# Optimization experiments

Measured on AMD Instinct MI355X. Metric: run time of the kernel, lower is better.

## Reference

```python
import jax, jax.numpy as jnp
import numpy as np

N_EMBD = 384
SEQ_LEN = 256
B = 512


def setup_inputs() -> dict:
    key = jax.random.key(0)
    ks = jax.random.split(key, 5)
    s = 1.0 / np.sqrt(N_EMBD)
    x = jax.random.normal(ks[0], (B, SEQ_LEN, N_EMBD), dtype=jnp.float32)
    W_qkv = jax.random.uniform(ks[1], (N_EMBD, 3 * N_EMBD), jnp.float32, -s, s)
    b_qkv = jax.random.uniform(ks[2], (3 * N_EMBD,), jnp.float32, -s, s)
    W_proj = jax.random.uniform(ks[3], (N_EMBD, N_EMBD), jnp.float32, -s, s)
    b_proj = jax.random.uniform(ks[4], (N_EMBD,), jnp.float32, -s, s)
    return {"x": x, "W_qkv": W_qkv, "b_qkv": b_qkv, "W_proj": W_proj, "b_proj": b_proj}


def reference(x, W_qkv, b_qkv, W_proj, b_proj):
    B_, T, C = x.shape
    qkv = jnp.einsum('btc,cd->btd', x, W_qkv) + b_qkv  # [B,T,3C]
    q, k, v = jnp.split(qkv, 3, axis=-1)
    # single-head attention, scaled by full embed dim C (as in source)
    att = jnp.einsum('btc,bsc->bts', q, k) / jnp.sqrt(jnp.float32(C))  # [B,T,T]
    causal = jnp.tril(jnp.ones((T, T), dtype=bool))
    att = jnp.where(causal, att, -jnp.inf)
    att = jax.nn.softmax(att, axis=-1)
    out = jnp.einsum('bts,bsc->btc', att, v)  # [B,T,C]
    return jnp.einsum('btc,cd->btd', out, W_proj) + b_proj
```

## Files before the change

kernel.cpp:

```cpp
#include <hip/hip_runtime.h>
#include <math.h>

#define TSEQ 256
#define CEMB 384
#define QK_LD 768
#define QKV_N 1152

typedef short short8 __attribute__((ext_vector_type(8)));
typedef short short4v __attribute__((ext_vector_type(4)));
typedef float f32x4 __attribute__((ext_vector_type(4)));

static __device__ __forceinline__ short f2bf(float f) {
    union { float f; unsigned u; } a;
    a.f = f;
    unsigned u = a.u + 0x7fffu + ((a.u >> 16) & 1u);
    return (short)(u >> 16);
}

static __device__ __forceinline__ void gload_lds16(const unsigned short* g,
                                                   unsigned short* l) {
    __builtin_amdgcn_global_load_lds(
        (const __attribute__((address_space(1))) unsigned int*)g,
        (__attribute__((address_space(3))) unsigned int*)l, 16, 0, 0);
}

__global__ __launch_bounds__(256) void cast_x_kernel(
    const float* __restrict__ x, unsigned short* __restrict__ xb, int n8)
{
    int i = blockIdx.x * 256 + threadIdx.x;
    const int stride = gridDim.x * 256;
    for (; i < n8; i += stride) {
        const float* s = x + (size_t)i * 8;
        float4 a = *(const float4*)(s);
        float4 c = *(const float4*)(s + 4);
        short8 o;
        o[0] = f2bf(a.x); o[1] = f2bf(a.y); o[2] = f2bf(a.z); o[3] = f2bf(a.w);
        o[4] = f2bf(c.x); o[5] = f2bf(c.y); o[6] = f2bf(c.z); o[7] = f2bf(c.w);
        *(short8*)(xb + (size_t)i * 8) = o;
    }
}

__global__ __launch_bounds__(256) void cast_wt_kernel(
    const float* __restrict__ W, unsigned short* __restrict__ Wt, int K, int N)
{
    int i = blockIdx.x * 256 + threadIdx.x;
    if (i < K * N) {
        int n = i / K;
        int k = i - n * K;
        Wt[i] = (unsigned short)f2bf(W[(size_t)k * N + n]);
    }
}

template <int MODE>
__global__ __launch_bounds__(256) void gemm_bf16_kernel(
    const unsigned short* __restrict__ A, const unsigned short* __restrict__ Bt,
    const float* __restrict__ bias, void* __restrict__ Cout,
    unsigned short* __restrict__ Vt, int M, int N, int K)
{
    __shared__ unsigned short As[2][128 * 32];
    __shared__ unsigned short Bs[2][128 * 32];

    const int tid  = threadIdx.x;
    const int wave = tid >> 6;
    const int lane = tid & 63;
    const int quad = lane >> 4;
    const int l16  = lane & 15;
    const int wr   = wave >> 1;
    const int wc   = wave & 1;

    const int gx  = gridDim.x;
    const int nwg = gridDim.x * gridDim.y;
    int bid = blockIdx.y * gx + blockIdx.x;
    if ((nwg & 7) == 0) bid = (bid & 7) * (nwg >> 3) + (bid >> 3);
    const int n0 = (bid % gx) * 128;
    const int m0 = (bid / gx) * 128;

    const int srow = tid >> 2;
    const int scol = (tid & 3) * 8;
    const unsigned short* Abase = A  + (size_t)(m0 + srow) * K + scol;
    const unsigned short* Bbase = Bt + (size_t)(n0 + srow) * K + scol;
    const int woff = wave << 9;

    f32x4 acc[4][4];
    #pragma unroll
    for (int mi = 0; mi < 4; ++mi)
        #pragma unroll
        for (int ni = 0; ni < 4; ++ni) acc[mi][ni] = (f32x4){0.f, 0.f, 0.f, 0.f};

    gload_lds16(Abase, &As[0][woff]);
    gload_lds16(Abase + (size_t)64 * K, &As[0][2048 + woff]);
    gload_lds16(Bbase, &Bs[0][woff]);
    gload_lds16(Bbase + (size_t)64 * K, &Bs[0][2048 + woff]);
    __syncthreads();

    int cur = 0;
    for (int kk = 32; kk < K; kk += 32) {
        gload_lds16(Abase + kk, &As[cur ^ 1][woff]);
        gload_lds16(Abase + (size_t)64 * K + kk, &As[cur ^ 1][2048 + woff]);
        gload_lds16(Bbase + kk, &Bs[cur ^ 1][woff]);
        gload_lds16(Bbase + (size_t)64 * K + kk, &Bs[cur ^ 1][2048 + woff]);

        short8 af[4], bfr[4];
        #pragma unroll
        for (int mi = 0; mi < 4; ++mi)
            af[mi] = *(const short8*)&As[cur][(wr * 64 + mi * 16 + l16) * 32 + quad * 8];
        #pragma unroll
        for (int ni = 0; ni < 4; ++ni)
            bfr[ni] = *(const short8*)&Bs[cur][(wc * 64 + ni * 16 + l16) * 32 + quad * 8];
        #pragma unroll
        for (int mi = 0; mi < 4; ++mi)
            #pragma unroll
            for (int ni = 0; ni < 4; ++ni)
                acc[mi][ni] = __builtin_amdgcn_mfma_f32_16x16x32_bf16(
                    af[mi], bfr[ni], acc[mi][ni], 0, 0, 0);

        __syncthreads();
        cur ^= 1;
    }
    {
        short8 af[4], bfr[4];
        #pragma unroll
        for (int mi = 0; mi < 4; ++mi)
            af[mi] = *(const short8*)&As[cur][(wr * 64 + mi * 16 + l16) * 32 + quad * 8];
        #pragma unroll
        for (int ni = 0; ni < 4; ++ni)
            bfr[ni] = *(const short8*)&Bs[cur][(wc * 64 + ni * 16 + l16) * 32 + quad * 8];
        #pragma unroll
        for (int mi = 0; mi < 4; ++mi)
            #pragma unroll
            for (int ni = 0; ni < 4; ++ni)
                acc[mi][ni] = __builtin_amdgcn_mfma_f32_16x16x32_bf16(
                    af[mi], bfr[ni], acc[mi][ni], 0, 0, 0);
    }

    if (MODE == 1 && n0 >= 768) {
        #pragma unroll
        for (int ni = 0; ni < 4; ++ni) {
            const int n = n0 + wc * 64 + ni * 16 + l16;
            const float bv = bias[n];
            const int c = n - 768;
            #pragma unroll
            for (int mi = 0; mi < 4; ++mi) {
                const int m = m0 + wr * 64 + mi * 16 + quad * 4;
                const int bb = m >> 8;
                const int t  = m & 255;
                short4v o;
                #pragma unroll
                for (int r = 0; r < 4; ++r)
                    o[r] = f2bf(acc[mi][ni][r] + bv);
                *(short4v*)(Vt + ((size_t)bb * CEMB + c) * TSEQ + t) = o;
            }
        }
        return;
    }

    #pragma unroll
    for (int ni = 0; ni < 4; ++ni) {
        const int n = n0 + wc * 64 + ni * 16 + l16;
        const float bv = bias[n];
        #pragma unroll
        for (int mi = 0; mi < 4; ++mi) {
            #pragma unroll
            for (int r = 0; r < 4; ++r) {
                const int m = m0 + wr * 64 + mi * 16 + quad * 4 + r;
                float v = acc[mi][ni][r] + bv;
                if (MODE == 1)
                    ((unsigned short*)Cout)[(size_t)m * QK_LD + n] = (unsigned short)f2bf(v);
                else
                    ((float*)Cout)[(size_t)m * N + n] = v;
            }
        }
    }
}

__global__ __launch_bounds__(64) void attn_mfma_kernel(
    const unsigned short* __restrict__ QKb, const unsigned short* __restrict__ Vt,
    unsigned short* __restrict__ Ob)
{
    const int nwg = gridDim.x;
    int bid = blockIdx.x;
    bid = (bid & 7) * (nwg >> 3) + (bid >> 3);
    const int b  = bid >> 4;
    const int st = bid & 15;

    const int lane = threadIdx.x;
    const int quad = lane >> 4;
    const int l16  = lane & 15;
    const int Q0   = st * 16;
    const int NT   = st + 1;
    const int NKT32  = (NT + 1) >> 1;
    const int kcnt   = NT * 16;
    const int padcnt = NKT32 * 32;

    __shared__ unsigned short Pw[16 * 264];

    const float scale = 0.051031036307982884f;

    const unsigned short* qbase = QKb + ((size_t)b * TSEQ + Q0) * QK_LD;
    short8 qf[12];
    #pragma unroll
    for (int f = 0; f < 12; ++f)
        qf[f] = *(const short8*)(qbase + (size_t)l16 * QK_LD + f * 32 + quad * 8);

    f32x4 s[16];
    #pragma unroll
    for (int t = 0; t < 16; ++t) s[t] = (f32x4){0.f, 0.f, 0.f, 0.f};

    const unsigned short* kB = QKb + (size_t)b * TSEQ * QK_LD + CEMB;
    #pragma unroll
    for (int t = 0; t < 16; ++t) {
        if (t <= st) {
            const unsigned short* kp = kB + (size_t)(t * 16 + l16) * QK_LD + quad * 8;
            #pragma unroll
            for (int f = 0; f < 12; ++f) {
                short8 kf = *(const short8*)(kp + f * 32);
                s[t] = __builtin_amdgcn_mfma_f32_16x16x32_bf16(qf[f], kf, s[t], 0, 0, 0);
            }
        }
    }

    float mt[4] = {-1e30f, -1e30f, -1e30f, -1e30f};
    #pragma unroll
    for (int t = 0; t < 16; ++t) {
        if (t <= st) {
            #pragma unroll
            for (int r = 0; r < 4; ++r) {
                const int qrow = Q0 + quad * 4 + r;
                float v = s[t][r] * scale;
                if (t * 16 + l16 > qrow) v = -1e30f;
                s[t][r] = v;
                mt[r] = fmaxf(mt[r], v);
            }
        }
    }
    #pragma unroll
    for (int off = 1; off <= 8; off <<= 1)
        #pragma unroll
        for (int r = 0; r < 4; ++r)
            mt[r] = fmaxf(mt[r], __shfl_xor(mt[r], off));

    float lr[4] = {0.f, 0.f, 0.f, 0.f};
    #pragma unroll
    for (int t = 0; t < 16; ++t) {
        if (t <= st) {
            #pragma unroll
            for (int r = 0; r < 4; ++r) {
                float p = __expf(s[t][r] - mt[r]);
                s[t][r] = p;
                lr[r] += p;
            }
        }
    }
    #pragma unroll
    for (int off = 1; off <= 8; off <<= 1)
        #pragma unroll
        for (int r = 0; r < 4; ++r)
            lr[r] += __shfl_xor(lr[r], off);
    float inv[4];
    #pragma unroll
    for (int r = 0; r < 4; ++r) inv[r] = 1.f / lr[r];

    #pragma unroll
    for (int t = 0; t < 16; ++t) {
        if (t * 16 < padcnt) {
            #pragma unroll
            for (int r = 0; r < 4; ++r) {
                float pv = (t <= st) ? s[t][r] : 0.f;
                Pw[(quad * 4 + r) * 264 + t * 16 + l16] = (unsigned short)f2bf(pv);
            }
        }
    }
    __asm__ __volatile__("s_waitcnt lgkmcnt(0)" ::: "memory");

    short8 pf[8];
    #pragma unroll
    for (int kt = 0; kt < 8; ++kt)
        if (kt < NKT32)
            pf[kt] = *(const short8*)(Pw + (size_t)l16 * 264 + kt * 32 + quad * 8);

    const unsigned short* vB = Vt + (size_t)b * CEMB * TSEQ;
    unsigned short* obase = Ob + ((size_t)b * TSEQ + Q0) * CEMB;
    #pragma unroll 4
    for (int ct = 0; ct < 24; ++ct) {
        const unsigned short* vp = vB + (size_t)(ct * 16 + l16) * TSEQ + quad * 8;
        f32x4 o = (f32x4){0.f, 0.f, 0.f, 0.f};
        #pragma unroll
        for (int kt = 0; kt < 8; ++kt) {
            if (kt < NKT32) {
                short8 vf = *(const short8*)(vp + kt * 32);
                o = __builtin_amdgcn_mfma_f32_16x16x32_bf16(pf[kt], vf, o, 0, 0, 0);
            }
        }
        #pragma unroll
        for (int r = 0; r < 4; ++r)
            obase[(size_t)(quad * 4 + r) * CEMB + ct * 16 + l16] =
                (unsigned short)f2bf(o[r] * inv[r]);
    }
}

extern "C" void kernel_launch(void* const* d_in, const int* in_sizes, int n_in,
                              void* d_out, int out_size, void* d_ws, size_t ws_size,
                              hipStream_t stream)
{
    const float* x      = (const float*)d_in[0];
    const float* W_qkv  = (const float*)d_in[1];
    const float* b_qkv  = (const float*)d_in[2];
    const float* W_proj = (const float*)d_in[3];
    const float* b_proj = (const float*)d_in[4];
    float* out = (float*)d_out;

    const int Btot = 512;
    const size_t xb_pb  = (size_t)TSEQ * CEMB * 2;
    const size_t qkb_pb = (size_t)TSEQ * QK_LD * 2;
    const size_t vt_pb  = (size_t)TSEQ * CEMB * 2;
    const size_t ob_pb  = (size_t)TSEQ * CEMB * 2;
    const size_t per_batch = xb_pb + qkb_pb + vt_pb + ob_pb;
    const size_t wq_sz = (size_t)CEMB * QKV_N * 2;
    const size_t wp_sz = (size_t)CEMB * CEMB * 2;
    const size_t fixed = wq_sz + wp_sz;

    size_t avail = (ws_size > fixed) ? (ws_size - fixed) : 0;
    int chunk = (int)(avail / per_batch);
    if (chunk > Btot) chunk = Btot;
    if (chunk < 1) chunk = 1;

    char* p = (char*)d_ws;
    unsigned short* xb  = (unsigned short*)p;  p += xb_pb * chunk;
    unsigned short* QKb = (unsigned short*)p;  p += qkb_pb * chunk;
    unsigned short* Vt  = (unsigned short*)p;  p += vt_pb * chunk;
    unsigned short* Ob  = (unsigned short*)p;  p += ob_pb * chunk;
    unsigned short* Wqt = (unsigned short*)p;  p += wq_sz;
    unsigned short* Wpt = (unsigned short*)p;

    cast_wt_kernel<<<(CEMB * QKV_N + 255) / 256, 256, 0, stream>>>(
        W_qkv, Wqt, CEMB, QKV_N);
    cast_wt_kernel<<<(CEMB * CEMB + 255) / 256, 256, 0, stream>>>(
        W_proj, Wpt, CEMB, CEMB);

    for (int b0 = 0; b0 < Btot; b0 += chunk) {
        int cb = (chunk < Btot - b0) ? chunk : (Btot - b0);
        int Mc = cb * TSEQ;

        int n8 = Mc * CEMB / 8;
        int gx = (n8 + 255) / 256;
        if (gx > 2048) gx = 2048;
        cast_x_kernel<<<gx, 256, 0, stream>>>(
            x + (size_t)b0 * TSEQ * CEMB, xb, n8);

        gemm_bf16_kernel<1><<<dim3(QKV_N / 128, Mc / 128), 256, 0, stream>>>(
            xb, Wqt, b_qkv, QKb, Vt, Mc, QKV_N, CEMB);

        attn_mfma_kernel<<<dim3(16 * cb), 64, 0, stream>>>(QKb, Vt, Ob);

        gemm_bf16_kernel<0><<<dim3(CEMB / 128, Mc / 128), 256, 0, stream>>>(
            Ob, Wpt, b_proj, out + (size_t)b0 * TSEQ * CEMB, nullptr, Mc, CEMB, CEMB);
    }
}
```

Measured before the change: 1.046 ms.

## Split fused attention into tiled QK GEMM, row softmax, and PV GEMM kernels

Replaces the single-wave per-16-row attention kernel with three kernels: a 128x128 LDS-tiled, double-buffered QK^T GEMM that skips the fully masked upper tile, a row softmax writing bf16 probabilities and inverse sums, and a tiled PV GEMM that limits K to the causal extent. The goal is better operand reuse through LDS and higher MFMA utilization than the old kernel, which reread K and V straight from global memory per 16-row tile. The cost is an fp32 score matrix and a bf16 P matrix round-tripping through global memory, plus extra launches and a smaller batch chunk from the larger workspace.

```diff
diff --git a/kernel.cpp b/kernel.cpp
--- a/kernel.cpp
+++ b/kernel.cpp
@@ -173,128 +173,242 @@
     }
 }
 
-__global__ __launch_bounds__(64) void attn_mfma_kernel(
-    const unsigned short* __restrict__ QKb, const unsigned short* __restrict__ Vt,
-    unsigned short* __restrict__ Ob)
-{
-    const int nwg = gridDim.x;
-    int bid = blockIdx.x;
-    bid = (bid & 7) * (nwg >> 3) + (bid >> 3);
-    const int b  = bid >> 4;
-    const int st = bid & 15;
-
-    const int lane = threadIdx.x;
+__global__ __launch_bounds__(256) void qk_gemm_kernel(
+    const unsigned short* __restrict__ QKb, float* __restrict__ S)
+{
+    const int tt = blockIdx.x;
+    const int b  = blockIdx.y;
+    const int ti = (tt >= 1) ? 1 : 0;
+    const int tj = (tt == 2) ? 1 : 0;
+    const int m0 = ti * 128, n0 = tj * 128;
+
+    __shared__ unsigned short As[2][128 * 32];
+    __shared__ unsigned short Bs[2][128 * 32];
+
+    const int tid  = threadIdx.x;
+    const int wave = tid >> 6;
+    const int lane = tid & 63;
     const int quad = lane >> 4;
     const int l16  = lane & 15;
-    const int Q0   = st * 16;
-    const int NT   = st + 1;
-    const int NKT32  = (NT + 1) >> 1;
-    const int kcnt   = NT * 16;
-    const int padcnt = NKT32 * 32;
-
-    __shared__ unsigned short Pw[16 * 264];
-
-    const float scale = 0.051031036307982884f;
-
-    const unsigned short* qbase = QKb + ((size_t)b * TSEQ + Q0) * QK_LD;
-    short8 qf[12];
-    #pragma unroll
-    for (int f = 0; f < 12; ++f)
-        qf[f] = *(const short8*)(qbase + (size_t)l16 * QK_LD + f * 32 + quad * 8);
-
-    f32x4 s[16];
-    #pragma unroll
-    for (int t = 0; t < 16; ++t) s[t] = (f32x4){0.f, 0.f, 0.f, 0.f};
-
-    const unsigned short* kB = QKb + (size_t)b * TSEQ * QK_LD + CEMB;
-    #pragma unroll
-    for (int t = 0; t < 16; ++t) {
-        if (t <= st) {
-            const unsigned short* kp = kB + (size_t)(t * 16 + l16) * QK_LD + quad * 8;
-            #pragma unroll
-            for (int f = 0; f < 12; ++f) {
-                short8 kf = *(const short8*)(kp + f * 32);
-                s[t] = __builtin_amdgcn_mfma_f32_16x16x32_bf16(qf[f], kf, s[t], 0, 0, 0);
+    const int wr   = wave >> 1;
+    const int wc   = wave & 1;
+
+    const int srow = tid >> 2;
+    const int scol = (tid & 3) * 8;
+    const unsigned short* Abase = QKb + ((size_t)b * TSEQ + m0 + srow) * QK_LD + scol;
+    const unsigned short* Bbase = QKb + ((size_t)b * TSEQ + n0 + srow) * QK_LD + CEMB + scol;
+    const int woff = wave << 9;
+
+    f32x4 acc[4][4];
+    #pragma unroll
+    for (int mi = 0; mi < 4; ++mi)
+        #pragma unroll
+        for (int ni = 0; ni < 4; ++ni) acc[mi][ni] = (f32x4){0.f, 0.f, 0.f, 0.f};
+
+    gload_lds16(Abase, &As[0][woff]);
+    gload_lds16(Abase + (size_t)64 * QK_LD, &As[0][2048 + woff]);
+    gload_lds16(Bbase, &Bs[0][woff]);
+    gload_lds16(Bbase + (size_t)64 * QK_LD, &Bs[0][2048 + woff]);
+    __syncthreads();
+
+    int cur = 0;
+    for (int kk = 32; kk < CEMB; kk += 32) {
+        gload_lds16(Abase + kk, &As[cur ^ 1][woff]);
+        gload_lds16(Abase + (size_t)64 * QK_LD + kk, &As[cur ^ 1][2048 + woff]);
+        gload_lds16(Bbase + kk, &Bs[cur ^ 1][woff]);
+        gload_lds16(Bbase + (size_t)64 * QK_LD + kk, &Bs[cur ^ 1][2048 + woff]);
+
+        short8 af[4], bfr[4];
+        #pragma unroll
+        for (int mi = 0; mi < 4; ++mi)
+            af[mi] = *(const short8*)&As[cur][(wr * 64 + mi * 16 + l16) * 32 + quad * 8];
+        #pragma unroll
+        for (int ni = 0; ni < 4; ++ni)
+            bfr[ni] = *(const short8*)&Bs[cur][(wc * 64 + ni * 16 + l16) * 32 + quad * 8];
+        #pragma unroll
+        for (int mi = 0; mi < 4; ++mi)
+            #pragma unroll
+            for (int ni = 0; ni < 4; ++ni)
+                acc[mi][ni] = __builtin_amdgcn_mfma_f32_16x16x32_bf16(
+                    af[mi], bfr[ni], acc[mi][ni], 0, 0, 0);
+
+        __syncthreads();
+        cur ^= 1;
+    }
+    {
+        short8 af[4], bfr[4];
+        #pragma unroll
+        for (int mi = 0; mi < 4; ++mi)
+            af[mi] = *(const short8*)&As[cur][(wr * 64 + mi * 16 + l16) * 32 + quad * 8];
+        #pragma unroll
+        for (int ni = 0; ni < 4; ++ni)
+            bfr[ni] = *(const short8*)&Bs[cur][(wc * 64 + ni * 16 + l16) * 32 + quad * 8];
+        #pragma unroll
+        for (int mi = 0; mi < 4; ++mi)
+            #pragma unroll
+            for (int ni = 0; ni < 4; ++ni)
+                acc[mi][ni] = __builtin_amdgcn_mfma_f32_16x16x32_bf16(
+                    af[mi], bfr[ni], acc[mi][ni], 0, 0, 0);
+    }
+
+    float* Sb = S + (size_t)b * TSEQ * TSEQ;
+    #pragma unroll
+    for (int ni = 0; ni < 4; ++ni) {
+        const int n = n0 + wc * 64 + ni * 16 + l16;
+        #pragma unroll
+        for (int mi = 0; mi < 4; ++mi) {
+            #pragma unroll
+            for (int r = 0; r < 4; ++r) {
+                const int m = m0 + wr * 64 + mi * 16 + quad * 4 + r;
+                Sb[(size_t)m * TSEQ + n] = acc[mi][ni][r];
             }
         }
     }
-
-    float mt[4] = {-1e30f, -1e30f, -1e30f, -1e30f};
-    #pragma unroll
-    for (int t = 0; t < 16; ++t) {
-        if (t <= st) {
-            #pragma unroll
-            for (int r = 0; r < 4; ++r) {
-                const int qrow = Q0 + quad * 4 + r;
-                float v = s[t][r] * scale;
-                if (t * 16 + l16 > qrow) v = -1e30f;
-                s[t][r] = v;
-                mt[r] = fmaxf(mt[r], v);
+}
+
+__global__ __launch_bounds__(256) void softmax_rows_kernel(
+    const float* __restrict__ S, unsigned short* __restrict__ P,
+    float* __restrict__ Linv)
+{
+    const int b    = blockIdx.y;
+    const int t    = blockIdx.x * 4 + (threadIdx.x >> 6);
+    const int lane = threadIdx.x & 63;
+    const int col  = lane * 4;
+    const int Kcov = ((t >> 7) + 1) * 128;
+    const float scale = 0.051031036307982884f;
+
+    const float* sp = S + ((size_t)b * TSEQ + t) * TSEQ;
+    float v[4];
+    if (col < Kcov) {
+        float4 sv = *(const float4*)(sp + col);
+        v[0] = (col + 0 <= t) ? sv.x * scale : -1e30f;
+        v[1] = (col + 1 <= t) ? sv.y * scale : -1e30f;
+        v[2] = (col + 2 <= t) ? sv.z * scale : -1e30f;
+        v[3] = (col + 3 <= t) ? sv.w * scale : -1e30f;
+    } else {
+        v[0] = v[1] = v[2] = v[3] = -1e30f;
+    }
+
+    float m = fmaxf(fmaxf(v[0], v[1]), fmaxf(v[2], v[3]));
+    #pragma unroll
+    for (int off = 1; off <= 32; off <<= 1)
+        m = fmaxf(m, __shfl_xor(m, off));
+
+    float p[4];
+    float s = 0.f;
+    #pragma unroll
+    for (int j = 0; j < 4; ++j) {
+        p[j] = __expf(v[j] - m);
+        s += p[j];
+    }
+    #pragma unroll
+    for (int off = 1; off <= 32; off <<= 1)
+        s += __shfl_xor(s, off);
+
+    if (lane == 0) Linv[(size_t)b * TSEQ + t] = 1.f / s;
+
+    if (col < Kcov) {
+        short4v o;
+        #pragma unroll
+        for (int j = 0; j < 4; ++j) o[j] = f2bf(p[j]);
+        *(short4v*)(P + ((size_t)b * TSEQ + t) * TSEQ + col) = o;
+    }
+}
+
+__global__ __launch_bounds__(256) void pv_gemm_kernel(
+    const unsigned short* __restrict__ P, const unsigned short* __restrict__ Vt,
+    const float* __restrict__ Linv, unsigned short* __restrict__ Ob)
+{
+    const int tt = blockIdx.x;
+    const int b  = blockIdx.y;
+    const int ti = tt / 3;
+    const int tj = tt - ti * 3;
+    const int m0 = ti * 128, n0 = tj * 128;
+    const int Kext = (ti + 1) * 128;
+
+    __shared__ unsigned short As[2][128 * 32];
+    __shared__ unsigned short Bs[2][128 * 32];
+
+    const int tid  = threadIdx.x;
+    const int wave = tid >> 6;
+    const int lane = tid & 63;
+    const int quad = lane >> 4;
+    const int l16  = lane & 15;
+    const int wr   = wave >> 1;
+    const int wc   = wave & 1;
+
+    const int srow = tid >> 2;
+    const int scol = (tid & 3) * 8;
+    const unsigned short* Abase = P  + ((size_t)b * TSEQ + m0 + srow) * TSEQ + scol;
+    const unsigned short* Bbase = Vt + ((size_t)b * CEMB + n0 + srow) * TSEQ + scol;
+    const int woff = wave << 9;
+
+    f32x4 acc[4][4];
+    #pragma unroll
+    for (int mi = 0; mi < 4; ++mi)
+        #pragma unroll
+        for (int ni = 0; ni < 4; ++ni) acc[mi][ni] = (f32x4){0.f, 0.f, 0.f, 0.f};
+
+    gload_lds16(Abase, &As[0][woff]);
+    gload_lds16(Abase + (size_t)64 * TSEQ, &As[0][2048 + woff]);
+    gload_lds16(Bbase, &Bs[0][woff]);
+    gload_lds16(Bbase + (size_t)64 * TSEQ, &Bs[0][2048 + woff]);
+    __syncthreads();
+
+    int cur = 0;
+    for (int kk = 32; kk < Kext; kk += 32) {
+        gload_lds16(Abase + kk, &As[cur ^ 1][woff]);
+        gload_lds16(Abase + (size_t)64 * TSEQ + kk, &As[cur ^ 1][2048 + woff]);
+        gload_lds16(Bbase + kk, &Bs[cur ^ 1][woff]);
+        gload_lds16(Bbase + (size_t)64 * TSEQ + kk, &Bs[cur ^ 1][2048 + woff]);
+
+        short8 af[4], bfr[4];
+        #pragma unroll
+        for (int mi = 0; mi < 4; ++mi)
+            af[mi] = *(const short8*)&As[cur][(wr * 64 + mi * 16 + l16) * 32 + quad * 8];
+        #pragma unroll
+        for (int ni = 0; ni < 4; ++ni)
+            bfr[ni] = *(const short8*)&Bs[cur][(wc * 64 + ni * 16 + l16) * 32 + quad * 8];
+        #pragma unroll
+        for (int mi = 0; mi < 4; ++mi)
+            #pragma unroll
+            for (int ni = 0; ni < 4; ++ni)
+                acc[mi][ni] = __builtin_amdgcn_mfma_f32_16x16x32_bf16(
+                    af[mi], bfr[ni], acc[mi][ni], 0, 0, 0);
+
+        __syncthreads();
+        cur ^= 1;
+    }
+    {
+        short8 af[4], bfr[4];
+        #pragma unroll
+        for (int mi = 0; mi < 4; ++mi)
+            af[mi] = *(const short8*)&As[cur][(wr * 64 + mi * 16 + l16) * 32 + quad * 8];
+        #pragma unroll
+        for (int ni = 0; ni < 4; ++ni)
+            bfr[ni] = *(const short8*)&Bs[cur][(wc * 64 + ni * 16 + l16) * 32 + quad * 8];
+        #pragma unroll
+        for (int mi = 0; mi < 4; ++mi)
+            #pragma unroll
+            for (int ni = 0; ni < 4; ++ni)
+                acc[mi][ni] = __builtin_amdgcn_mfma_f32_16x16x32_bf16(
+                    af[mi], bfr[ni], acc[mi][ni], 0, 0, 0);
+    }
+
+    const float* lv = Linv + (size_t)b * TSEQ;
+    unsigned short* ob = Ob + (size_t)b * TSEQ * CEMB;
+    #pragma unroll
+    for (int mi = 0; mi < 4; ++mi) {
+        #pragma unroll
+        for (int r = 0; r < 4; ++r) {
+            const int m = m0 + wr * 64 + mi * 16 + quad * 4 + r;
+            const float inv = lv[m];
+            #pragma unroll
+            for (int ni = 0; ni < 4; ++ni) {
+                const int n = n0 + wc * 64 + ni * 16 + l16;
+                ob[(size_t)m * CEMB + n] = (unsigned short)f2bf(acc[mi][ni][r] * inv);
             }
         }
-    }
-    #pragma unroll
-    for (int off = 1; off <= 8; off <<= 1)
-        #pragma unroll
-        for (int r = 0; r < 4; ++r)
-            mt[r] = fmaxf(mt[r], __shfl_xor(mt[r], off));
-
-    float lr[4] = {0.f, 0.f, 0.f, 0.f};
-    #pragma unroll
-    for (int t = 0; t < 16; ++t) {
-        if (t <= st) {
-            #pragma unroll
-            for (int r = 0; r < 4; ++r) {
-                float p = __expf(s[t][r] - mt[r]);
-                s[t][r] = p;
-                lr[r] += p;
-            }
-        }
-    }
-    #pragma unroll
-    for (int off = 1; off <= 8; off <<= 1)
-        #pragma unroll
-        for (int r = 0; r < 4; ++r)
-            lr[r] += __shfl_xor(lr[r], off);
-    float inv[4];
-    #pragma unroll
-    for (int r = 0; r < 4; ++r) inv[r] = 1.f / lr[r];
-
-    #pragma unroll
-    for (int t = 0; t < 16; ++t) {
-        if (t * 16 < padcnt) {
-            #pragma unroll
-            for (int r = 0; r < 4; ++r) {
-                float pv = (t <= st) ? s[t][r] : 0.f;
-                Pw[(quad * 4 + r) * 264 + t * 16 + l16] = (unsigned short)f2bf(pv);
-            }
-        }
-    }
-    __asm__ __volatile__("s_waitcnt lgkmcnt(0)" ::: "memory");
-
-    short8 pf[8];
-    #pragma unroll
-    for (int kt = 0; kt < 8; ++kt)
-        if (kt < NKT32)
-            pf[kt] = *(const short8*)(Pw + (size_t)l16 * 264 + kt * 32 + quad * 8);
-
-    const unsigned short* vB = Vt + (size_t)b * CEMB * TSEQ;
-    unsigned short* obase = Ob + ((size_t)b * TSEQ + Q0) * CEMB;
-    #pragma unroll 4
-    for (int ct = 0; ct < 24; ++ct) {
-        const unsigned short* vp = vB + (size_t)(ct * 16 + l16) * TSEQ + quad * 8;
-        f32x4 o = (f32x4){0.f, 0.f, 0.f, 0.f};
-        #pragma unroll
-        for (int kt = 0; kt < 8; ++kt) {
-            if (kt < NKT32) {
-                short8 vf = *(const short8*)(vp + kt * 32);
-                o = __builtin_amdgcn_mfma_f32_16x16x32_bf16(pf[kt], vf, o, 0, 0, 0);
-            }
-        }
-        #pragma unroll
-        for (int r = 0; r < 4; ++r)
-            obase[(size_t)(quad * 4 + r) * CEMB + ct * 16 + l16] =
-                (unsigned short)f2bf(o[r] * inv[r]);
     }
 }
 
@@ -310,11 +424,14 @@
     float* out = (float*)d_out;
 
     const int Btot = 512;
-    const size_t xb_pb  = (size_t)TSEQ * CEMB * 2;
-    const size_t qkb_pb = (size_t)TSEQ * QK_LD * 2;
-    const size_t vt_pb  = (size_t)TSEQ * CEMB * 2;
-    const size_t ob_pb  = (size_t)TSEQ * CEMB * 2;
-    const size_t per_batch = xb_pb + qkb_pb + vt_pb + ob_pb;
+    const size_t xb_pb   = (size_t)TSEQ * CEMB * 2;
+    const size_t qkb_pb  = (size_t)TSEQ * QK_LD * 2;
+    const size_t vt_pb   = (size_t)TSEQ * CEMB * 2;
+    const size_t ob_pb   = (size_t)TSEQ * CEMB * 2;
+    const size_t s_pb    = (size_t)TSEQ * TSEQ * 4;
+    const size_t p_pb    = (size_t)TSEQ * TSEQ * 2;
+    const size_t linv_pb = (size_t)TSEQ * 4;
+    const size_t per_batch = xb_pb + qkb_pb + vt_pb + ob_pb + s_pb + p_pb + linv_pb;
     const size_t wq_sz = (size_t)CEMB * QKV_N * 2;
     const size_t wp_sz = (size_t)CEMB * CEMB * 2;
     const size_t fixed = wq_sz + wp_sz;
@@ -323,14 +440,18 @@
     int chunk = (int)(avail / per_batch);
     if (chunk > Btot) chunk = Btot;
     if (chunk < 1) chunk = 1;
+    if (chunk >= 8) chunk -= chunk % 8;
 
     char* p = (char*)d_ws;
-    unsigned short* xb  = (unsigned short*)p;  p += xb_pb * chunk;
-    unsigned short* QKb = (unsigned short*)p;  p += qkb_pb * chunk;
-    unsigned short* Vt  = (unsigned short*)p;  p += vt_pb * chunk;
-    unsigned short* Ob  = (unsigned short*)p;  p += ob_pb * chunk;
-    unsigned short* Wqt = (unsigned short*)p;  p += wq_sz;
-    unsigned short* Wpt = (unsigned short*)p;
+    unsigned short* xb   = (unsigned short*)p;  p += xb_pb * chunk;
+    unsigned short* QKb  = (unsigned short*)p;  p += qkb_pb * chunk;
+    unsigned short* Vt   = (unsigned short*)p;  p += vt_pb * chunk;
+    unsigned short* Ob   = (unsigned short*)p;  p += ob_pb * chunk;
+    float*          Sbuf = (float*)p;           p += s_pb * chunk;
+    unsigned short* Pbuf = (unsigned short*)p;  p += p_pb * chunk;
+    float*          Linv = (float*)p;           p += linv_pb * chunk;
+    unsigned short* Wqt  = (unsigned short*)p;  p += wq_sz;
+    unsigned short* Wpt  = (unsigned short*)p;
 
     cast_wt_kernel<<<(CEMB * QKV_N + 255) / 256, 256, 0, stream>>>(
         W_qkv, Wqt, CEMB, QKV_N);
@@ -350,7 +471,11 @@
         gemm_bf16_kernel<1><<<dim3(QKV_N / 128, Mc / 128), 256, 0, stream>>>(
             xb, Wqt, b_qkv, QKb, Vt, Mc, QKV_N, CEMB);
 
-        attn_mfma_kernel<<<dim3(16 * cb), 64, 0, stream>>>(QKb, Vt, Ob);
+        qk_gemm_kernel<<<dim3(3, cb), 256, 0, stream>>>(QKb, Sbuf);
+
+        softmax_rows_kernel<<<dim3(64, cb), 256, 0, stream>>>(Sbuf, Pbuf, Linv);
+
+        pv_gemm_kernel<<<dim3(6, cb), 256, 0, stream>>>(Pbuf, Vt, Linv, Ob);
 
         gemm_bf16_kernel<0><<<dim3(CEMB / 128, Mc / 128), 256, 0, stream>>>(
             Ob, Wpt, b_proj, out + (size_t)b0 * TSEQ * CEMB, nullptr, Mc, CEMB, CEMB);
```

New measurement: 873.6 us. 1.2x faster.
